# Optimization experiments

Measured on AMD Instinct MI355X. Metric: run time of the kernel, lower is better.

Reference implementation:

```python
import jax, jax.numpy as jnp
import numpy as np

T = 2048
HID = 2048
H = 16
NOPE = 128
ROPE = 64
QKD = NOPE + ROPE  # 192
VD = 128
QLR = 1536
KVLR = 512
IDX_H = 32
IDX_D = 128
TOPK = 512
EPS = 1e-6
SCALING = QKD ** -0.5


def rms_norm(x, w):
    return x * jax.lax.rsqrt(jnp.mean(x * x, axis=-1, keepdims=True) + EPS) * w


def layer_norm(x, g, b):
    mu = jnp.mean(x, axis=-1, keepdims=True)
    var = jnp.mean((x - mu) ** 2, axis=-1, keepdims=True)
    return (x - mu) * jax.lax.rsqrt(var + EPS) * g + b


def apply_rope(x, positions, base=10000.0):
    # non-neox (interleaved) rotary; x: [..., d] with leading token axis
    d = x.shape[-1]
    inv = 1.0 / (base ** (jnp.arange(0, d, 2, dtype=jnp.float32) / d))
    f = positions.astype(jnp.float32)[:, None] * inv  # [T, d/2]
    shp = (x.shape[0],) + (1,) * (x.ndim - 2) + (d // 2,)
    cos, sin = jnp.cos(f).reshape(shp), jnp.sin(f).reshape(shp)
    x1, x2 = x[..., ::2], x[..., 1::2]
    return jnp.stack([x1 * cos - x2 * sin, x1 * sin + x2 * cos], axis=-1).reshape(x.shape)


def setup_inputs() -> dict:
    key = jax.random.key(0)
    ks = jax.random.split(key, 10)
    s = 0.02
    return {
        "positions": jnp.arange(T, dtype=jnp.int64) if jax.config.jax_enable_x64 else jnp.arange(T, dtype=jnp.int32),
        "hidden_states": jax.random.normal(ks[0], (T, HID), jnp.float32),
        "w_qkv_a": jax.random.normal(ks[1], (HID, QLR + KVLR + ROPE), jnp.float32) * s,
        "q_a_ln_w": jnp.ones((QLR,), jnp.float32),
        "w_qb": jax.random.normal(ks[2], (QLR, H * QKD), jnp.float32) * s,
        "kv_a_ln_w": jnp.ones((KVLR,), jnp.float32),
        "w_kvb": jax.random.normal(ks[3], (KVLR, H * (NOPE + VD)), jnp.float32) * s,
        "w_o": jax.random.normal(ks[4], (H * VD, HID), jnp.float32) * s,
        "w_idx_qb": jax.random.normal(ks[5], (QLR, IDX_H * IDX_D), jnp.float32) * s,
        "w_idx_k": jax.random.normal(ks[6], (HID, IDX_D), jnp.float32) * s,
        "idx_k_gamma": jnp.ones((IDX_D,), jnp.float32),
        "idx_k_beta": jnp.zeros((IDX_D,), jnp.float32),
        "w_wproj": jax.random.normal(ks[7], (HID, IDX_H), jnp.float32) * s,
        "b_wproj": jnp.zeros((IDX_H,), jnp.float32),
    }


def _forward(positions, hidden_states, w_qkv_a, q_a_ln_w, w_qb, kv_a_ln_w, w_kvb,
             w_o, w_idx_qb, w_idx_k, idx_k_gamma, idx_k_beta, w_wproj, b_wproj):
    t = hidden_states.shape[0]
    # fused low-rank projections
    qkv = hidden_states @ w_qkv_a
    q_c, kv_c, k_pe = jnp.split(qkv, [QLR, QLR + KVLR], axis=-1)
    q_c = rms_norm(q_c, q_a_ln_w)           # hidden_states_or_q_c
    kv_cn = rms_norm(kv_c, kv_a_ln_w)

    # ---- Indexer (lightning top-k token selection) ----
    qi = (q_c @ w_idx_qb).reshape(t, IDX_H, IDX_D)
    qi_pe, qi_nope = qi[..., :ROPE], qi[..., ROPE:]
    ki = layer_norm(hidden_states @ w_idx_k, idx_k_gamma, idx_k_beta)  # [T, IDX_D]
    ki_pe, ki_nope = ki[..., :ROPE], ki[..., ROPE:]
    qi = jnp.concatenate([apply_rope(qi_pe, positions), qi_nope], axis=-1)
    ki = jnp.concatenate([apply_rope(ki_pe, positions), ki_nope], axis=-1)
    w = (hidden_states @ w_wproj + b_wproj) * (IDX_D ** -0.5) * (IDX_H ** -0.5)  # [T, IDX_H]
    logits = jax.nn.relu(jnp.einsum('thd,sd->ths', qi, ki))   # [T, IDX_H, T]
    score = jnp.einsum('th,ths->ts', w, logits)               # [T, T]
    causal = jnp.tril(jnp.ones((t, t), bool))
    neg = jnp.finfo(score.dtype).min
    score = jnp.where(causal, score, neg)
    _, topk_idx = jax.lax.top_k(score, TOPK)                  # [T, TOPK]
    sel = jnp.zeros((t, t), bool).at[jnp.arange(t)[:, None], topk_idx].set(True)
    mask = causal & sel

    # ---- MLA attention ----
    q = (q_c @ w_qb).reshape(t, H, QKD)
    q_nope, q_pe = q[..., :NOPE], q[..., NOPE:]
    q_pe = apply_rope(q_pe, positions)
    k_pe_r = apply_rope(k_pe, positions)                      # [T, ROPE], shared across heads
    kv = (kv_cn @ w_kvb).reshape(t, H, NOPE + VD)
    k_nope, v = kv[..., :NOPE], kv[..., NOPE:]
    q_full = jnp.concatenate([q_nope, q_pe], axis=-1)         # [T, H, QKD]
    k_full = jnp.concatenate([k_nope, jnp.broadcast_to(k_pe_r[:, None, :], (t, H, ROPE))], axis=-1)
    attn = jnp.einsum('thd,shd->hts', q_full, k_full) * SCALING
    attn = jnp.where(mask[None], attn, neg)
    p = jax.nn.softmax(attn, axis=-1)
    out = jnp.einsum('hts,shv->thv', p, v).reshape(t, H * VD)
    return out @ w_o


def reference(positions, hidden_states, w_qkv_a, q_a_ln_w, w_qb, kv_a_ln_w, w_kvb,
              w_o, w_idx_qb, w_idx_k, idx_k_gamma, idx_k_beta, w_wproj, b_wproj):
    return _forward(positions, hidden_states, w_qkv_a, q_a_ln_w, w_qb, kv_a_ln_w,
                    w_kvb, w_o, w_idx_qb, w_idx_k, idx_k_gamma, idx_k_beta,
                    w_wproj, b_wproj)
```

## Files before the change

### kernel.cpp

```cpp
#include <hip/hip_runtime.h>
#include <cfloat>
#include <cmath>

#define T_    2048
#define HID_  2048
#define QKVN_ 2112
#define QKVX_ 2272
#define QLR_  1536
#define KVLR_ 512
#define ROPE_ 64
#define NOPE_ 128
#define QKD_  192
#define VD_   128
#define H_    16
#define IDXH_ 32
#define IDXD_ 128
#define TOPK_ 512
#define EPS_  1e-6f
#define SCALING_ 0.07216878364870323f

typedef unsigned int u32;
typedef unsigned short u16;
typedef __bf16 bf16x8 __attribute__((ext_vector_type(8)));
typedef _Float16 f16;
typedef f16 f16x8 __attribute__((ext_vector_type(8)));
typedef float f32x4 __attribute__((ext_vector_type(4)));

__device__ __forceinline__ u16 f2bf(float x) {
  u32 u = __float_as_uint(x);
  u32 r = (u + 0x7fffu + ((u >> 16) & 1u)) >> 16;
  return (u16)r;
}
__device__ __forceinline__ float bf2f(u16 h) { return __uint_as_float(((u32)h) << 16); }
__device__ __forceinline__ u32 pack2(float a, float b) { return (u32)f2bf(a) | ((u32)f2bf(b) << 16); }
__device__ __forceinline__ bf16x8 ld8(const void* p) { return *(const bf16x8*)p; }
__device__ __forceinline__ f32x4 mfma16(bf16x8 a, bf16x8 b, f32x4 c) {
  return __builtin_amdgcn_mfma_f32_16x16x32_bf16(a, b, c, 0, 0, 0);
}
__device__ __forceinline__ u16 hbits(f16 h) { union { f16 h; u16 u; } c; c.h = h; return c.u; }
__device__ __forceinline__ u32 hpack(f16 a, f16 b) { return (u32)hbits(a) | ((u32)hbits(b) << 16); }
__device__ __forceinline__ f16x8 ldh8(const void* p) { return *(const f16x8*)p; }
__device__ __forceinline__ f32x4 mfmah(f16x8 a, f16x8 b, f32x4 c) {
  return __builtin_amdgcn_mfma_f32_16x16x32_f16(a, b, c, 0, 0, 0);
}
__device__ __forceinline__ void gload16(const u16* g, u16* l) {
  __builtin_amdgcn_global_load_lds(
      (__attribute__((address_space(1))) void*)(g),
      (__attribute__((address_space(3))) void*)(l), 16, 0, 0);
}

struct TSJob { const float* src; u16* oh; u16* ol; int K; int N; };
__global__ __launch_bounds__(256) void transpose_split_multi(
    TSJob j0, TSJob j1, TSJob j2, TSJob j3) {
  TSJob jb = (blockIdx.z == 0) ? j0 : (blockIdx.z == 1) ? j1 : (blockIdx.z == 2) ? j2 : j3;
  int k0 = blockIdx.y * 64, n0 = blockIdx.x * 64;
  if (k0 >= jb.K || n0 >= jb.N) return;
  __shared__ float t[64][65];
  for (int j = 0; j < 16; ++j) {
    int u = threadIdx.x + 256 * j; int r = u >> 6, c = u & 63;
    t[r][c] = (k0 + r < jb.K && n0 + c < jb.N) ? jb.src[(size_t)(k0 + r) * jb.N + n0 + c] : 0.f;
  }
  __syncthreads();
  for (int j = 0; j < 16; ++j) {
    int u = threadIdx.x + 256 * j; int r = u >> 6, c = u & 63;
    if (n0 + r < jb.N && k0 + c < jb.K) {
      float v = t[c][r];
      f16 h = (f16)v;
      jb.oh[(size_t)(n0 + r) * jb.K + k0 + c] = hbits(h);
      jb.ol[(size_t)(n0 + r) * jb.K + k0 + c] = hbits((f16)(v - (float)h));
    }
  }
}

struct TBJob { const float* src; u16* out; int K; int N; };
__global__ __launch_bounds__(256) void transpose_bf16_multi(TBJob j0, TBJob j1, TBJob j2) {
  TBJob jb = (blockIdx.z == 0) ? j0 : (blockIdx.z == 1) ? j1 : j2;
  int k0 = blockIdx.y * 64, n0 = blockIdx.x * 64;
  if (k0 >= jb.K || n0 >= jb.N) return;
  __shared__ float t[64][65];
  for (int j = 0; j < 16; ++j) {
    int u = threadIdx.x + 256 * j; int r = u >> 6, c = u & 63;
    t[r][c] = (k0 + r < jb.K && n0 + c < jb.N) ? jb.src[(size_t)(k0 + r) * jb.N + n0 + c] : 0.f;
  }
  __syncthreads();
  for (int j = 0; j < 16; ++j) {
    int u = threadIdx.x + 256 * j; int r = u >> 6, c = u & 63;
    if (n0 + r < jb.N && k0 + c < jb.K) jb.out[(size_t)(n0 + r) * jb.K + k0 + c] = f2bf(t[c][r]);
  }
}

__global__ __launch_bounds__(256) void split_f16_k(
    const float* __restrict__ in, u16* __restrict__ hi, u16* __restrict__ lo, long n) {
  for (long i = ((long)blockIdx.x * 256 + threadIdx.x) * 4; i < n; i += (long)gridDim.x * 1024) {
    float4 v = *(const float4*)(in + i);
    f16 a = (f16)v.x, b = (f16)v.y, c = (f16)v.z, d = (f16)v.w;
    *(u32*)(hi + i) = hpack(a, b);
    *(u32*)(hi + i + 2) = hpack(c, d);
    *(u32*)(lo + i) = hpack((f16)(v.x - (float)a), (f16)(v.y - (float)b));
    *(u32*)(lo + i + 2) = hpack((f16)(v.z - (float)c), (f16)(v.w - (float)d));
  }
}

__global__ __launch_bounds__(256) void conv_bf16_k(
    const float* __restrict__ in, u16* __restrict__ out, long n) {
  for (long i = ((long)blockIdx.x * 256 + threadIdx.x) * 4; i < n; i += (long)gridDim.x * 1024) {
    float4 v = *(const float4*)(in + i);
    *(u32*)(out + i) = pack2(v.x, v.y);
    *(u32*)(out + i + 2) = pack2(v.z, v.w);
  }
}

__global__ __launch_bounds__(256) void gemm_hl(
    const u16* __restrict__ Ah_, const u16* __restrict__ Al_, int lda,
    const u16* __restrict__ Bh_, const u16* __restrict__ Bl_, int ldb,
    float* __restrict__ C, int ldc, const float* __restrict__ bias, int bcol0,
    float bscale, int N, int K) {
  __shared__ u32 Ah[128][16], Al[128][16], Bh[128][16], Bl[128][16];
  const int tid = threadIdx.x;
  const int bm = blockIdx.y * 128, bn = blockIdx.x * 128;
  const int wid = tid >> 6, lane = tid & 63, wr = wid >> 1, wc = wid & 1;
  const int lr = lane & 15, lg = lane >> 4;
  const u16* srcb = (wid == 0) ? Ah_ : (wid == 1) ? Al_ : (wid == 2) ? Bh_ : Bl_;
  const int sld = (wid < 2) ? lda : ldb;
  const int rb = (wid < 2) ? bm : bn;
  u16* dst = (u16*)((wid == 0) ? &Ah[0][0] : (wid == 1) ? &Al[0][0]
                                           : (wid == 2) ? &Bh[0][0] : &Bl[0][0]);
  const int rowl = lane >> 2;
  const int offl = (lane & 3) * 8;
  f32x4 acc[4][4] = {};
  for (int k0 = 0; k0 < K; k0 += 32) {
#pragma unroll
    for (int c = 0; c < 8; ++c) {
      int gr = rb + c * 16 + rowl;
      if (wid >= 2) gr = min(gr, N - 1);
      gload16(srcb + (size_t)gr * sld + k0 + offl, dst + c * 512);
    }
    __syncthreads();
    f16x8 ah[4], al[4], bh[4], bl[4];
#pragma unroll
    for (int i = 0; i < 4; ++i) {
      ah[i] = ldh8(&Ah[wr * 64 + i * 16 + lr][lg * 4]);
      al[i] = ldh8(&Al[wr * 64 + i * 16 + lr][lg * 4]);
      bh[i] = ldh8(&Bh[wc * 64 + i * 16 + lr][lg * 4]);
      bl[i] = ldh8(&Bl[wc * 64 + i * 16 + lr][lg * 4]);
    }
#pragma unroll
    for (int i = 0; i < 4; ++i)
#pragma unroll
      for (int jn = 0; jn < 4; ++jn) {
        acc[i][jn] = mfmah(ah[i], bh[jn], acc[i][jn]);
        acc[i][jn] = mfmah(ah[i], bl[jn], acc[i][jn]);
        acc[i][jn] = mfmah(al[i], bh[jn], acc[i][jn]);
      }
    __syncthreads();
  }
#pragma unroll
  for (int i = 0; i < 4; ++i)
#pragma unroll
    for (int jn = 0; jn < 4; ++jn)
#pragma unroll
      for (int j = 0; j < 4; ++j) {
        int row = bm + wr * 64 + i * 16 + lg * 4 + j;
        int col = bn + wc * 64 + jn * 16 + lr;
        if (col < N) {
          float v = acc[i][jn][j];
          if (col >= bcol0) v = (v + bias[col - bcol0]) * bscale;
          C[(size_t)row * ldc + col] = v;
        }
      }
}

template <int CBF16>
__global__ __launch_bounds__(256) void gemm_t(
    const u16* __restrict__ Ab, int lda, long aoz,
    const u16* __restrict__ Bt, int ldb, long boz,
    void* __restrict__ Cp, int ldc, long coz, int N, int K) {
  __shared__ u32 As[128][16], Bs[128][16];
  const int tid = threadIdx.x;
  const int z = blockIdx.z;
  const int bm = blockIdx.y * 128, bn = blockIdx.x * 128;
  const int wid = tid >> 6, lane = tid & 63, wr = wid >> 1, wc = wid & 1;
  const int lr = lane & 15, lg = lane >> 4;
  const u16* A = Ab + aoz * z;
  const u16* B = Bt + boz * z;
  const u16* srcb = (wid < 2) ? A : B;
  const int sld = (wid < 2) ? lda : ldb;
  const int rb = (wid < 2) ? bm : bn;
  u16* dst = (u16*)((wid < 2) ? &As[0][0] : &Bs[0][0]);
  const int ccb = (wid & 1) * 4;
  const int rowl = lane >> 2;
  const int offl = (lane & 3) * 8;
  f32x4 acc[4][4] = {};
  for (int k0 = 0; k0 < K; k0 += 32) {
#pragma unroll
    for (int c = 0; c < 4; ++c) {
      int cc = ccb + c;
      int gr = rb + cc * 16 + rowl;
      if (wid >= 2) gr = min(gr, N - 1);
      gload16(srcb + (size_t)gr * sld + k0 + offl, dst + cc * 512);
    }
    __syncthreads();
    bf16x8 af[4], bf[4];
#pragma unroll
    for (int i = 0; i < 4; ++i) {
      af[i] = ld8(&As[wr * 64 + i * 16 + lr][lg * 4]);
      bf[i] = ld8(&Bs[wc * 64 + i * 16 + lr][lg * 4]);
    }
#pragma unroll
    for (int i = 0; i < 4; ++i)
#pragma unroll
      for (int jn = 0; jn < 4; ++jn)
        acc[i][jn] = mfma16(af[i], bf[jn], acc[i][jn]);
    __syncthreads();
  }
#pragma unroll
  for (int i = 0; i < 4; ++i)
#pragma unroll
    for (int jn = 0; jn < 4; ++jn)
#pragma unroll
      for (int j = 0; j < 4; ++j) {
        int row = bm + wr * 64 + i * 16 + lg * 4 + j;
        int col = bn + wc * 64 + jn * 16 + lr;
        if (col < N) {
          if (CBF16) ((u16*)Cp)[coz * z + (size_t)row * ldc + col] = f2bf(acc[i][jn][j]);
          else ((float*)Cp)[coz * z + (size_t)row * ldc + col] = acc[i][jn][j];
        }
      }
}

__global__ __launch_bounds__(256) void rmsnorm_kernel(
    const float* __restrict__ qkvx, const float* __restrict__ qw,
    const float* __restrict__ kvw, u16* __restrict__ qcb,
    u16* __restrict__ qch, u16* __restrict__ qcl, u16* __restrict__ kv_cn) {
  const int t = blockIdx.x, tid = threadIdx.x;
  const float* row = qkvx + (size_t)t * QKVX_;
  __shared__ float red[256];
  float ss = 0.f;
  for (int i = tid; i < QLR_; i += 256) { float v = row[i]; ss += v * v; }
  red[tid] = ss; __syncthreads();
  for (int s = 128; s; s >>= 1) { if (tid < s) red[tid] += red[tid + s]; __syncthreads(); }
  float scl = 1.0f / sqrtf(red[0] / (float)QLR_ + EPS_);
  for (int i = tid; i < QLR_; i += 256) {
    float val = row[i] * scl * qw[i];
    qcb[(size_t)t * QLR_ + i] = f2bf(val);
    f16 h = (f16)val;
    qch[(size_t)t * QLR_ + i] = hbits(h);
    qcl[(size_t)t * QLR_ + i] = hbits((f16)(val - (float)h));
  }
  __syncthreads();
  ss = 0.f;
  for (int i = tid; i < KVLR_; i += 256) { float v = row[QLR_ + i]; ss += v * v; }
  red[tid] = ss; __syncthreads();
  for (int s = 128; s; s >>= 1) { if (tid < s) red[tid] += red[tid + s]; __syncthreads(); }
  scl = 1.0f / sqrtf(red[0] / (float)KVLR_ + EPS_);
  for (int i = tid; i < KVLR_; i += 256)
    kv_cn[(size_t)t * KVLR_ + i] = f2bf(row[QLR_ + i] * scl * kvw[i]);
}

__device__ __forceinline__ void rope_pair(float pos, int j, float& x0, float& x1) {
  float inv = powf(10000.f, -(float)j * (1.f / 32.f));
  float f = pos * inv;
  float c = cosf(f), s = sinf(f);
  float a = x0, b = x1;
  x0 = a * c - b * s;
  x1 = a * s + b * c;
}

__global__ __launch_bounds__(256) void rope_qi_split_kernel(
    const float* __restrict__ qi, u16* __restrict__ qih, u16* __restrict__ qil) {
  const int t = blockIdx.x, tid = threadIdx.x;
  float pos = (float)t;
  const float* src = qi + (size_t)t * (IDXH_ * IDXD_);
  u16* dh = qih + (size_t)t * (IDXH_ * IDXD_);
  u16* dl = qil + (size_t)t * (IDXH_ * IDXD_);
  for (int p = tid; p < IDXH_ * IDXD_ / 2; p += 256) {
    int d = p & 63;
    float x0 = src[2 * p], x1 = src[2 * p + 1];
    if (d < 32) rope_pair(pos, d, x0, x1);
    f16 h0 = (f16)x0, h1 = (f16)x1;
    *(u32*)(dh + 2 * p) = hpack(h0, h1);
    *(u32*)(dl + 2 * p) = hpack((f16)(x0 - (float)h0), (f16)(x1 - (float)h1));
  }
}

__global__ __launch_bounds__(256) void rope_q_bf_kernel(u16* __restrict__ qfb) {
  const int t = blockIdx.x, tid = threadIdx.x;
  float pos = (float)t;
  for (int idx = tid; idx < H_ * 32; idx += 256) {
    int hh = idx / 32, j = idx % 32;
    u16* p = qfb + (size_t)t * (H_ * QKD_) + hh * QKD_ + NOPE_ + 2 * j;
    float x0 = bf2f(p[0]), x1 = bf2f(p[1]);
    rope_pair(pos, j, x0, x1);
    p[0] = f2bf(x0); p[1] = f2bf(x1);
  }
}

__global__ __launch_bounds__(64) void rope_kpe_kernel(
    const float* __restrict__ qkvx, u16* __restrict__ kper) {
  const int t = blockIdx.x, tid = threadIdx.x;
  if (tid >= 32) return;
  float pos = (float)t;
  const float* p = qkvx + (size_t)t * QKVX_ + (QLR_ + KVLR_);
  float x0 = p[2 * tid], x1 = p[2 * tid + 1];
  rope_pair(pos, tid, x0, x1);
  kper[(size_t)t * ROPE_ + 2 * tid] = f2bf(x0);
  kper[(size_t)t * ROPE_ + 2 * tid + 1] = f2bf(x1);
}

__global__ __launch_bounds__(128) void ki_ln_rope_kernel(
    const float* __restrict__ qkvx, const float* __restrict__ gamma,
    const float* __restrict__ beta, u16* __restrict__ kih, u16* __restrict__ kil) {
  const int t = blockIdx.x, tid = threadIdx.x;
  __shared__ float x[128];
  __shared__ float red[128];
  float v = qkvx[(size_t)t * QKVX_ + QKVN_ + tid];
  red[tid] = v; __syncthreads();
  for (int s = 64; s; s >>= 1) { if (tid < s) red[tid] += red[tid + s]; __syncthreads(); }
  float mu = red[0] / 128.f;
  __syncthreads();
  float d = v - mu;
  red[tid] = d * d; __syncthreads();
  for (int s = 64; s; s >>= 1) { if (tid < s) red[tid] += red[tid + s]; __syncthreads(); }
  float var = red[0] / 128.f;
  float y = d * (1.0f / sqrtf(var + EPS_)) * gamma[tid] + beta[tid];
  x[tid] = y; __syncthreads();
  float pos = (float)t;
  if (tid < 32) {
    float x0 = x[2 * tid], x1 = x[2 * tid + 1];
    rope_pair(pos, tid, x0, x1);
    x[2 * tid] = x0; x[2 * tid + 1] = x1;
  }
  __syncthreads();
  float fv = x[tid];
  f16 h = (f16)fv;
  kih[(size_t)t * IDXD_ + tid] = hbits(h);
  kil[(size_t)t * IDXD_ + tid] = hbits((f16)(fv - (float)h));
}

__global__ __launch_bounds__(256) void score_mfma(
    const u16* __restrict__ qih, const u16* __restrict__ qil,
    const u16* __restrict__ kih, const u16* __restrict__ kil,
    const float* __restrict__ wgt, int ldw, float* __restrict__ score) {
  const int s0 = blockIdx.x * 64, t0 = blockIdx.y * 64;
  if (s0 > t0 + 63) return;
  __shared__ u32 Kh[64][68], Kl[64][68], Qh[64][68], Ql[64][68];
  __shared__ float wts[64][33];
  const int tid = threadIdx.x;
  const int wid = tid >> 6, lane = tid & 63, wr = wid >> 1, wc = wid & 1;
  const int lr = lane & 15, lg = lane >> 4;
#pragma unroll
  for (int j = 0; j < 4; ++j) {
    int u = tid + 256 * j; int row = u >> 4, p = u & 15;
    *(uint4*)&Kh[row][p * 4] = *(const uint4*)(kih + (size_t)(s0 + row) * IDXD_ + p * 8);
    *(uint4*)&Kl[row][p * 4] = *(const uint4*)(kil + (size_t)(s0 + row) * IDXD_ + p * 8);
  }
#pragma unroll
  for (int j = 0; j < 8; ++j) {
    int u = tid + 256 * j; int r = u >> 5, c = u & 31;
    wts[r][c] = wgt[(size_t)(t0 + r) * ldw + c];
  }
  __syncthreads();
  f16x8 bh[2][4], bl[2][4];
#pragma unroll
  for (int ni = 0; ni < 2; ++ni)
#pragma unroll
    for (int kb = 0; kb < 4; ++kb) {
      bh[ni][kb] = ldh8(&Kh[wc * 32 + ni * 16 + lr][kb * 16 + lg * 4]);
      bl[ni][kb] = ldh8(&Kl[wc * 32 + ni * 16 + lr][kb * 16 + lg * 4]);
    }
  f32x4 fin[2][2] = {};
  for (int h = 0; h < IDXH_; ++h) {
#pragma unroll
    for (int j = 0; j < 4; ++j) {
      int u = tid + 256 * j; int row = u >> 4, p = u & 15;
      size_t g = (size_t)(t0 + row) * (IDXH_ * IDXD_) + h * IDXD_ + p * 8;
      *(uint4*)&Qh[row][p * 4] = *(const uint4*)(qih + g);
      *(uint4*)&Ql[row][p * 4] = *(const uint4*)(qil + g);
    }
    __syncthreads();
    f32x4 acch[2][2] = {};
#pragma unroll
    for (int kb = 0; kb < 4; ++kb) {
      f16x8 ah0 = ldh8(&Qh[wr * 32 + lr][kb * 16 + lg * 4]);
      f16x8 ah1 = ldh8(&Qh[wr * 32 + 16 + lr][kb * 16 + lg * 4]);
      f16x8 al0 = ldh8(&Ql[wr * 32 + lr][kb * 16 + lg * 4]);
      f16x8 al1 = ldh8(&Ql[wr * 32 + 16 + lr][kb * 16 + lg * 4]);
#pragma unroll
      for (int ni = 0; ni < 2; ++ni) {
        acch[0][ni] = mfmah(ah0, bh[ni][kb], acch[0][ni]);
        acch[0][ni] = mfmah(ah0, bl[ni][kb], acch[0][ni]);
        acch[0][ni] = mfmah(al0, bh[ni][kb], acch[0][ni]);
        acch[1][ni] = mfmah(ah1, bh[ni][kb], acch[1][ni]);
        acch[1][ni] = mfmah(ah1, bl[ni][kb], acch[1][ni]);
        acch[1][ni] = mfmah(al1, bh[ni][kb], acch[1][ni]);
      }
    }
#pragma unroll
    for (int mi = 0; mi < 2; ++mi)
#pragma unroll
      for (int j = 0; j < 4; ++j) {
        float w = wts[wr * 32 + mi * 16 + lg * 4 + j][h];
        fin[mi][0][j] += w * fmaxf(acch[mi][0][j], 0.f);
        fin[mi][1][j] += w * fmaxf(acch[mi][1][j], 0.f);
      }
    __syncthreads();
  }
#pragma unroll
  for (int mi = 0; mi < 2; ++mi)
#pragma unroll
    for (int ni = 0; ni < 2; ++ni)
#pragma unroll
      for (int j = 0; j < 4; ++j) {
        int row = t0 + wr * 32 + mi * 16 + lg * 4 + j;
        int col = s0 + wc * 32 + ni * 16 + lr;
        score[(size_t)row * T_ + col] = fin[mi][ni][j];
      }
}

__global__ __launch_bounds__(256) void topk_kernel(
    const float* __restrict__ score, int* __restrict__ selidx,
    int* __restrict__ selcnt) {
  const int t = blockIdx.x;
  const int L = t + 1;
  const int tid = threadIdx.x;
  if (L <= TOPK_) {
    for (int j = tid; j < TOPK_; j += 256)
      selidx[(size_t)t * TOPK_ + j] = (j < L) ? j : 0;
    if (tid == 0) selcnt[t] = L;
    return;
  }
  __shared__ unsigned u[T_];
  __shared__ unsigned hist[16];
  __shared__ unsigned sprefix;
  __shared__ int sk;
  __shared__ int part[256];
  for (int i = tid; i < T_; i += 256) {
    float v = (i < L) ? score[(size_t)t * T_ + i] : -FLT_MAX;
    unsigned b = __float_as_uint(v);
    u[i] = (b & 0x80000000u) ? ~b : (b | 0x80000000u);
  }
  if (tid == 0) { sprefix = 0u; sk = TOPK_; }
  __syncthreads();
  for (int pass = 0; pass < 8; ++pass) {
    const int shift = 28 - 4 * pass;
    if (tid < 16) hist[tid] = 0u;
    __syncthreads();
    unsigned pfx = sprefix;
    for (int i = tid; i < L; i += 256) {
      unsigned val = u[i];
      bool match = (pass == 0) || ((val >> (shift + 4)) == pfx);
      if (match) atomicAdd(&hist[(val >> shift) & 15u], 1u);
    }
    __syncthreads();
    if (tid == 0) {
      int k = sk; unsigned cum = 0u; int bsel = 0;
      for (int bb = 15; bb >= 0; --bb) {
        if (cum + hist[bb] >= (unsigned)k) { bsel = bb; sk = k - (int)cum; break; }
        cum += hist[bb];
      }
      sprefix = (sprefix << 4) | (unsigned)bsel;
    }
    __syncthreads();
  }
  const unsigned thr = sprefix;
  const int kEq = sk;
  const int base = tid * 8;
  int eqloc[8]; int esum = 0;
  for (int r = 0; r < 8; ++r) {
    int i = base + r;
    int f = (i < L && u[i] == thr) ? 1 : 0;
    eqloc[r] = esum; esum += f;
  }
  part[tid] = esum; __syncthreads();
  for (int off = 1; off < 256; off <<= 1) {
    int v = (tid >= off) ? part[tid - off] : 0;
    __syncthreads();
    part[tid] += v;
    __syncthreads();
  }
  const int ebase = (tid > 0) ? part[tid - 1] : 0;
  __syncthreads();
  int sloc[8], selflag[8]; int ssum = 0;
  for (int r = 0; r < 8; ++r) {
    int i = base + r;
    int f = 0;
    if (i < L) {
      unsigned ui = u[i];
      if (ui > thr) f = 1;
      else if (ui == thr && (ebase + eqloc[r]) < kEq) f = 1;
    }
    selflag[r] = f; sloc[r] = ssum; ssum += f;
  }
  part[tid] = ssum; __syncthreads();
  for (int off = 1; off < 256; off <<= 1) {
    int v = (tid >= off) ? part[tid - off] : 0;
    __syncthreads();
    part[tid] += v;
    __syncthreads();
  }
  const int sbase = (tid > 0) ? part[tid - 1] : 0;
  for (int r = 0; r < 8; ++r)
    if (selflag[r]) selidx[(size_t)t * TOPK_ + sbase + sloc[r]] = base + r;
  if (tid == 0) selcnt[t] = TOPK_;
}

__global__ __launch_bounds__(256, 3) void attn_mla_kernel(
    const u16* __restrict__ qeff, const u16* __restrict__ qfb,
    const u16* __restrict__ kvcn, const u16* __restrict__ kper,
    const int* __restrict__ selidx, const int* __restrict__ selcnt,
    u16* __restrict__ Olat) {
  const int t = blockIdx.x;
  const int tid = threadIdx.x;
  const int wid = tid >> 6, lane = tid & 63;
  const int lr = lane & 15, lg = lane >> 4;
  __shared__ int sidxs[512];
  __shared__ u16 Pb[16][520];
  __shared__ u32 Vp[4][16][128];
  __shared__ float redm[4][16];
  __shared__ float reds[4][16];
  const int cnt = selcnt[t];
  for (int j = tid; j < 512; j += 256) sidxs[j] = selidx[(size_t)t * TOPK_ + j];
  __syncthreads();

  int srow[8];
  const u16* kb8[8];
  const u16* kp8[8];
#pragma unroll
  for (int m = 0; m < 8; ++m) {
    srow[m] = sidxs[wid * 128 + m * 16 + lr];
    kb8[m] = kvcn + (size_t)srow[m] * 512 + lg * 8;
    kp8[m] = kper + (size_t)srow[m] * 64 + lg * 8;
  }
  const u16* qe = qeff + (size_t)t * (H_ * 512) + lr * 512 + lg * 8;
  const u16* qp = qfb + (size_t)t * (H_ * QKD_) + lr * QKD_ + NOPE_ + lg * 8;
  f32x4 lgv[8] = {};
  bf16x8 kc[8];
#pragma unroll
  for (int m = 0; m < 8; ++m) kc[m] = ld8(kb8[m]);
#pragma unroll
  for (int kb = 0; kb < 16; ++kb) {
    bf16x8 qfk = ld8(qe + kb * 32);
    bf16x8 kn[8];
#pragma unroll
    for (int m = 0; m < 8; ++m)
      kn[m] = (kb < 15) ? ld8(kb8[m] + (kb + 1) * 32) : ld8(kp8[m]);
#pragma unroll
    for (int m = 0; m < 8; ++m) lgv[m] = mfma16(kc[m], qfk, lgv[m]);
#pragma unroll
    for (int m = 0; m < 8; ++m) kc[m] = kn[m];
  }
  {
    bf16x8 qfk = ld8(qp);
    bf16x8 kn[8];
#pragma unroll
    for (int m = 0; m < 8; ++m) kn[m] = ld8(kp8[m] + 32);
#pragma unroll
    for (int m = 0; m < 8; ++m) lgv[m] = mfma16(kc[m], qfk, lgv[m]);
#pragma unroll
    for (int m = 0; m < 8; ++m) kc[m] = kn[m];
  }
  {
    bf16x8 qfk = ld8(qp + 32);
#pragma unroll
    for (int m = 0; m < 8; ++m) lgv[m] = mfma16(kc[m], qfk, lgv[m]);
  }

  float mx = -FLT_MAX;
#pragma unroll
  for (int m = 0; m < 8; ++m)
#pragma unroll
    for (int j = 0; j < 4; ++j) {
      int slot = wid * 128 + m * 16 + lg * 4 + j;
      float v = (slot < cnt) ? lgv[m][j] * SCALING_ : -FLT_MAX;
      lgv[m][j] = v;
      mx = fmaxf(mx, v);
    }
  mx = fmaxf(mx, __shfl_xor(mx, 16));
  mx = fmaxf(mx, __shfl_xor(mx, 32));
  if (lane < 16) redm[wid][lane] = mx;
  __syncthreads();
  float hm = fmaxf(fmaxf(redm[0][lr], redm[1][lr]), fmaxf(redm[2][lr], redm[3][lr]));
  float sm = 0.f;
#pragma unroll
  for (int m = 0; m < 8; ++m)
#pragma unroll
    for (int j = 0; j < 4; ++j) {
      int slot = wid * 128 + m * 16 + lg * 4 + j;
      float e = (slot < cnt) ? expf(lgv[m][j] - hm) : 0.f;
      lgv[m][j] = e; sm += e;
    }
  sm += __shfl_xor(sm, 16);
  sm += __shfl_xor(sm, 32);
  if (lane < 16) reds[wid][lane] = sm;
  __syncthreads();
  float inv = 1.f / (reds[0][lr] + reds[1][lr] + reds[2][lr] + reds[3][lr]);
#pragma unroll
  for (int m = 0; m < 8; ++m) {
    int sl = wid * 128 + m * 16 + lg * 4;
    *(u32*)&Pb[lr][sl] = pack2(lgv[m][0] * inv, lgv[m][1] * inv);
    *(u32*)&Pb[lr][sl + 2] = pack2(lgv[m][2] * inv, lgv[m][3] * inv);
  }
  __syncthreads();

  const int pl = lane >> 4;
  const int gq = lane & 15;
  const u16* vsrc = kvcn + wid * 128 + gq * 8;
  f32x4 oacc[8] = {};
  uint4 ra[4], rb[4];
#pragma unroll
  for (int s = 0; s < 4; ++s) {
    int p = s * 4 + pl;
    ra[s] = *(const uint4*)(vsrc + (size_t)sidxs[2 * p] * 512);
    rb[s] = *(const uint4*)(vsrc + (size_t)sidxs[2 * p + 1] * 512);
  }
  for (int c = 0; c < 16; ++c) {
#pragma unroll
    for (int s = 0; s < 4; ++s) {
      int p = s * 4 + pl;
      int col = (gq * 8) ^ ((s & 3) << 3);
      const u16* A = (const u16*)&ra[s];
      const u16* B = (const u16*)&rb[s];
      u32 w[8];
#pragma unroll
      for (int j = 0; j < 8; ++j) w[j] = (u32)A[j] | ((u32)B[j] << 16);
      *(uint4*)&Vp[wid][p][col] = make_uint4(w[0], w[1], w[2], w[3]);
      *(uint4*)&Vp[wid][p][col + 4] = make_uint4(w[4], w[5], w[6], w[7]);
    }
    if (c < 15) {
#pragma unroll
      for (int s = 0; s < 4; ++s) {
        int p = s * 4 + pl;
        ra[s] = *(const uint4*)(vsrc + (size_t)sidxs[(c + 1) * 32 + 2 * p] * 512);
        rb[s] = *(const uint4*)(vsrc + (size_t)sidxs[(c + 1) * 32 + 2 * p + 1] * 512);
      }
    }
    bf16x8 pa = ld8(&Pb[lr][c * 32 + lg * 8]);
    union BB { u32 u[4]; bf16x8 v; };
    BB bb[8];
#pragma unroll
    for (int C = 0; C < 8; ++C) {
      int col = (C * 16 + lr) ^ (lg << 3);
#pragma unroll
      for (int e = 0; e < 4; ++e)
        bb[C].u[e] = Vp[wid][lg * 4 + e][col];
    }
    __builtin_amdgcn_s_setprio(1);
#pragma unroll
    for (int C = 0; C < 8; ++C) oacc[C] = mfma16(pa, bb[C].v, oacc[C]);
    __builtin_amdgcn_s_setprio(0);
  }
#pragma unroll
  for (int C = 0; C < 8; ++C)
#pragma unroll
    for (int j = 0; j < 4; ++j) {
      int h = lg * 4 + j;
      Olat[(size_t)t * (H_ * 512) + h * 512 + wid * 128 + C * 16 + lr] = f2bf(oacc[C][j]);
    }
}

extern "C" void kernel_launch(void* const* d_in, const int* in_sizes, int n_in,
                              void* d_out, int out_size, void* d_ws, size_t ws_size,
                              hipStream_t stream) {
  const float* hidden    = (const float*)d_in[1];
  const float* w_qkv_a   = (const float*)d_in[2];
  const float* q_a_ln_w  = (const float*)d_in[3];
  const float* w_qb      = (const float*)d_in[4];
  const float* kv_a_ln_w = (const float*)d_in[5];
  const float* w_kvb     = (const float*)d_in[6];
  const float* w_o       = (const float*)d_in[7];
  const float* w_idx_qb  = (const float*)d_in[8];
  const float* w_idx_k   = (const float*)d_in[9];
  const float* idx_g     = (const float*)d_in[10];
  const float* idx_b     = (const float*)d_in[11];
  const float* w_wproj   = (const float*)d_in[12];
  const float* b_wproj   = (const float*)d_in[13];

  char* W = (char*)d_ws;
  size_t o = 0;
  auto alloc = [&](size_t bytes) { void* p = W + o; o += (bytes + 255) & ~(size_t)255; return p; };
  u16* qcb     = (u16*)alloc((size_t)T_ * QLR_ * 2);
  u16* kv_cn   = (u16*)alloc((size_t)T_ * KVLR_ * 2);
  u16* kper    = (u16*)alloc((size_t)T_ * ROPE_ * 2);
  int* selidx  = (int*)alloc((size_t)T_ * TOPK_ * 4);
  int* selcnt  = (int*)alloc((size_t)T_ * 4);
  u16* kih     = (u16*)alloc((size_t)T_ * IDXD_ * 2);
  u16* kil     = (u16*)alloc((size_t)T_ * IDXD_ * 2);
  u16* hidh    = (u16*)alloc((size_t)T_ * HID_ * 2);
  u16* hidl    = (u16*)alloc((size_t)T_ * HID_ * 2);
  u16* qch     = (u16*)alloc((size_t)T_ * QLR_ * 2);
  u16* qcl     = (u16*)alloc((size_t)T_ * QLR_ * 2);
  u16* wiqh    = (u16*)alloc((size_t)(IDXH_ * IDXD_) * QLR_ * 2);
  u16* wiql    = (u16*)alloc((size_t)(IDXH_ * IDXD_) * QLR_ * 2);
  u16* qih     = qch;
  u16* qil     = qch + (size_t)T_ * IDXH_ * IDXD_;
  float* qi    = (float*)alloc((size_t)T_ * IDXH_ * IDXD_ * 4);
  u16* qeff    = (u16*)qi;
  float* score = (float*)alloc((size_t)T_ * T_ * 4);
  u16* qfb     = (u16*)score;
  u16* attno   = (u16*)score;
  u16* wcath   = (u16*)alloc((size_t)QKVX_ * HID_ * 2);
  u16* wcatl   = (u16*)alloc((size_t)QKVX_ * HID_ * 2);
  float* qkvx  = (float*)alloc((size_t)T_ * QKVX_ * 4);
  u16* Olat    = wcath;
  u16* wqbt    = (u16*)alloc((size_t)(H_ * QKD_) * QLR_ * 2);
  u16* wkvb    = (u16*)alloc((size_t)KVLR_ * (H_ * 256) * 2);
  u16* wkvbt   = (u16*)alloc((size_t)(H_ * 256) * KVLR_ * 2);
  u16* wot     = (u16*)alloc((size_t)(H_ * VD_) * HID_ * 2);

  dim3 blk(256);
  auto g2 = [](int M, int N, int Z) { return dim3((N + 127) / 128, M / 128, Z); };

  {
    TSJob j0{w_qkv_a, wcath, wcatl, HID_, QKVN_};
    TSJob j1{w_idx_qb, wiqh, wiql, QLR_, IDXH_ * IDXD_};
    TSJob j2{w_idx_k, wcath + (size_t)QKVN_ * HID_, wcatl + (size_t)QKVN_ * HID_, HID_, IDXD_};
    TSJob j3{w_wproj, wcath + (size_t)(QKVN_ + IDXD_) * HID_, wcatl + (size_t)(QKVN_ + IDXD_) * HID_, HID_, IDXH_};
    transpose_split_multi<<<dim3(64, 32, 4), blk, 0, stream>>>(j0, j1, j2, j3);
  }
  {
    TBJob j0{w_qb, wqbt, QLR_, H_ * QKD_};
    TBJob j1{w_kvb, wkvbt, KVLR_, H_ * 256};
    TBJob j2{w_o, wot, H_ * VD_, HID_};
    transpose_bf16_multi<<<dim3(64, 32, 3), blk, 0, stream>>>(j0, j1, j2);
  }
  split_f16_k<<<2048, blk, 0, stream>>>(hidden, hidh, hidl, (long)T_ * HID_);
  conv_bf16_k<<<2048, blk, 0, stream>>>(w_kvb, wkvb, (long)KVLR_ * H_ * 256);

  gemm_hl<<<g2(T_, QKVX_, 1), blk, 0, stream>>>(
      hidh, hidl, HID_, wcath, wcatl, HID_, qkvx, QKVX_,
      b_wproj, QKVN_ + IDXD_, 0.015625f, QKVX_, HID_);
  rmsnorm_kernel<<<T_, blk, 0, stream>>>(qkvx, q_a_ln_w, kv_a_ln_w, qcb, qch, qcl, kv_cn);
  rope_kpe_kernel<<<T_, 64, 0, stream>>>(qkvx, kper);
  ki_ln_rope_kernel<<<T_, 128, 0, stream>>>(qkvx, idx_g, idx_b, kih, kil);

  gemm_hl<<<g2(T_, IDXH_ * IDXD_, 1), blk, 0, stream>>>(
      qch, qcl, QLR_, wiqh, wiql, QLR_, qi, IDXH_ * IDXD_,
      nullptr, 1 << 30, 1.f, IDXH_ * IDXD_, QLR_);
  rope_qi_split_kernel<<<T_, blk, 0, stream>>>(qi, qih, qil);

  score_mfma<<<dim3(32, 32), blk, 0, stream>>>(qih, qil, kih, kil,
                                               qkvx + QKVN_ + IDXD_, QKVX_, score);
  topk_kernel<<<T_, blk, 0, stream>>>(score, selidx, selcnt);

  gemm_t<1><<<g2(T_, H_ * QKD_, 1), blk, 0, stream>>>(qcb, QLR_, 0, wqbt, QLR_, 0, qfb, H_ * QKD_, 0, H_ * QKD_, QLR_);
  rope_q_bf_kernel<<<T_, blk, 0, stream>>>(qfb);
  gemm_t<1><<<g2(T_, 512, H_), blk, 0, stream>>>(qfb, H_ * QKD_, QKD_, wkvb, H_ * 256, 256, qeff, H_ * 512, 512, 512, NOPE_);
  attn_mla_kernel<<<T_, blk, 0, stream>>>(qeff, qfb, kv_cn, kper, selidx, selcnt, Olat);
  gemm_t<1><<<g2(T_, VD_, H_), blk, 0, stream>>>(Olat, H_ * 512, 512, wkvbt + 128 * 512, KVLR_, 256 * 512, attno, H_ * VD_, VD_, VD_, 512);
  gemm_t<0><<<g2(T_, HID_, 1), blk, 0, stream>>>(attno, H_ * VD_, 0, wot, H_ * VD_, 0, d_out, HID_, 0, HID_, H_ * VD_);
}
```

Measured before the change: 712.5 us.

## Precompute RoPE cos/sin table and stage attention keys through LDS

Adds a kernel that precomputes a per-position cos/sin table once, and the four RoPE kernels now read from it instead of calling powf/sinf/cosf per element. Separately, the MLA attention score loop now gathers each selected key row into shared memory with global_load_lds, waits on it, then reads MFMA operands from LDS, and preloads all query fragments into registers. The shared buffer is reused for the V staging. The key gather was previously register-pipelined, while the new version waits on vmcnt(0) every k-block, which serialises load and compute and uses more registers for the query fragments.

```diff
diff --git a/kernel.cpp b/kernel.cpp
--- a/kernel.cpp
+++ b/kernel.cpp
@@ -47,6 +47,20 @@
   __builtin_amdgcn_global_load_lds(
       (__attribute__((address_space(1))) void*)(g),
       (__attribute__((address_space(3))) void*)(l), 16, 0, 0);
+}
+
+__global__ __launch_bounds__(256) void rope_tab_kernel(float2* __restrict__ tab) {
+  int i = blockIdx.x * 256 + threadIdx.x;
+  if (i >= T_ * 32) return;
+  int t = i >> 5, j = i & 31;
+  float inv = powf(10000.f, -(float)j * (1.f / 32.f));
+  float f = (float)t * inv;
+  tab[i] = make_float2(cosf(f), sinf(f));
+}
+__device__ __forceinline__ void rope_apply(float2 cs, float& x0, float& x1) {
+  float a = x0, b = x1;
+  x0 = a * cs.x - b * cs.y;
+  x1 = a * cs.y + b * cs.x;
 }
 
 struct TSJob { const float* src; u16* oh; u16* ol; int K; int N; };
@@ -257,59 +271,51 @@
     kv_cn[(size_t)t * KVLR_ + i] = f2bf(row[QLR_ + i] * scl * kvw[i]);
 }
 
-__device__ __forceinline__ void rope_pair(float pos, int j, float& x0, float& x1) {
-  float inv = powf(10000.f, -(float)j * (1.f / 32.f));
-  float f = pos * inv;
-  float c = cosf(f), s = sinf(f);
-  float a = x0, b = x1;
-  x0 = a * c - b * s;
-  x1 = a * s + b * c;
-}
-
 __global__ __launch_bounds__(256) void rope_qi_split_kernel(
-    const float* __restrict__ qi, u16* __restrict__ qih, u16* __restrict__ qil) {
+    const float* __restrict__ qi, const float2* __restrict__ tab,
+    u16* __restrict__ qih, u16* __restrict__ qil) {
   const int t = blockIdx.x, tid = threadIdx.x;
-  float pos = (float)t;
   const float* src = qi + (size_t)t * (IDXH_ * IDXD_);
   u16* dh = qih + (size_t)t * (IDXH_ * IDXD_);
   u16* dl = qil + (size_t)t * (IDXH_ * IDXD_);
   for (int p = tid; p < IDXH_ * IDXD_ / 2; p += 256) {
     int d = p & 63;
     float x0 = src[2 * p], x1 = src[2 * p + 1];
-    if (d < 32) rope_pair(pos, d, x0, x1);
+    if (d < 32) rope_apply(tab[t * 32 + d], x0, x1);
     f16 h0 = (f16)x0, h1 = (f16)x1;
     *(u32*)(dh + 2 * p) = hpack(h0, h1);
     *(u32*)(dl + 2 * p) = hpack((f16)(x0 - (float)h0), (f16)(x1 - (float)h1));
   }
 }
 
-__global__ __launch_bounds__(256) void rope_q_bf_kernel(u16* __restrict__ qfb) {
+__global__ __launch_bounds__(256) void rope_q_bf_kernel(
+    u16* __restrict__ qfb, const float2* __restrict__ tab) {
   const int t = blockIdx.x, tid = threadIdx.x;
-  float pos = (float)t;
   for (int idx = tid; idx < H_ * 32; idx += 256) {
     int hh = idx / 32, j = idx % 32;
     u16* p = qfb + (size_t)t * (H_ * QKD_) + hh * QKD_ + NOPE_ + 2 * j;
     float x0 = bf2f(p[0]), x1 = bf2f(p[1]);
-    rope_pair(pos, j, x0, x1);
+    rope_apply(tab[t * 32 + j], x0, x1);
     p[0] = f2bf(x0); p[1] = f2bf(x1);
   }
 }
 
 __global__ __launch_bounds__(64) void rope_kpe_kernel(
-    const float* __restrict__ qkvx, u16* __restrict__ kper) {
+    const float* __restrict__ qkvx, const float2* __restrict__ tab,
+    u16* __restrict__ kper) {
   const int t = blockIdx.x, tid = threadIdx.x;
   if (tid >= 32) return;
-  float pos = (float)t;
   const float* p = qkvx + (size_t)t * QKVX_ + (QLR_ + KVLR_);
   float x0 = p[2 * tid], x1 = p[2 * tid + 1];
-  rope_pair(pos, tid, x0, x1);
+  rope_apply(tab[t * 32 + tid], x0, x1);
   kper[(size_t)t * ROPE_ + 2 * tid] = f2bf(x0);
   kper[(size_t)t * ROPE_ + 2 * tid + 1] = f2bf(x1);
 }
 
 __global__ __launch_bounds__(128) void ki_ln_rope_kernel(
     const float* __restrict__ qkvx, const float* __restrict__ gamma,
-    const float* __restrict__ beta, u16* __restrict__ kih, u16* __restrict__ kil) {
+    const float* __restrict__ beta, const float2* __restrict__ tab,
+    u16* __restrict__ kih, u16* __restrict__ kil) {
   const int t = blockIdx.x, tid = threadIdx.x;
   __shared__ float x[128];
   __shared__ float red[128];
@@ -324,10 +330,9 @@
   float var = red[0] / 128.f;
   float y = d * (1.0f / sqrtf(var + EPS_)) * gamma[tid] + beta[tid];
   x[tid] = y; __syncthreads();
-  float pos = (float)t;
   if (tid < 32) {
     float x0 = x[2 * tid], x1 = x[2 * tid + 1];
-    rope_pair(pos, tid, x0, x1);
+    rope_apply(tab[t * 32 + tid], x0, x1);
     x[2 * tid] = x0; x[2 * tid + 1] = x1;
   }
   __syncthreads();
@@ -515,54 +520,49 @@
   const int lr = lane & 15, lg = lane >> 4;
   __shared__ int sidxs[512];
   __shared__ u16 Pb[16][520];
-  __shared__ u32 Vp[4][16][128];
+  __shared__ u16 SB[4][4096];
   __shared__ float redm[4][16];
   __shared__ float reds[4][16];
   const int cnt = selcnt[t];
   for (int j = tid; j < 512; j += 256) sidxs[j] = selidx[(size_t)t * TOPK_ + j];
   __syncthreads();
 
-  int srow[8];
-  const u16* kb8[8];
-  const u16* kp8[8];
-#pragma unroll
-  for (int m = 0; m < 8; ++m) {
-    srow[m] = sidxs[wid * 128 + m * 16 + lr];
-    kb8[m] = kvcn + (size_t)srow[m] * 512 + lg * 8;
-    kp8[m] = kper + (size_t)srow[m] * 64 + lg * 8;
-  }
+  const int kl = lane >> 2;
+  const int pc = (lane & 3) * 8;
+  int skey[8];
+#pragma unroll
+  for (int j = 0; j < 8; ++j) skey[j] = sidxs[wid * 128 + j * 16 + kl];
+  u16* ksw = &SB[wid][0];
+
   const u16* qe = qeff + (size_t)t * (H_ * 512) + lr * 512 + lg * 8;
   const u16* qp = qfb + (size_t)t * (H_ * QKD_) + lr * QKD_ + NOPE_ + lg * 8;
+  bf16x8 qf[18];
+#pragma unroll
+  for (int kb = 0; kb < 16; ++kb) qf[kb] = ld8(qe + kb * 32);
+  qf[16] = ld8(qp);
+  qf[17] = ld8(qp + 32);
+
   f32x4 lgv[8] = {};
-  bf16x8 kc[8];
-#pragma unroll
-  for (int m = 0; m < 8; ++m) kc[m] = ld8(kb8[m]);
-#pragma unroll
-  for (int kb = 0; kb < 16; ++kb) {
-    bf16x8 qfk = ld8(qe + kb * 32);
-    bf16x8 kn[8];
-#pragma unroll
-    for (int m = 0; m < 8; ++m)
-      kn[m] = (kb < 15) ? ld8(kb8[m] + (kb + 1) * 32) : ld8(kp8[m]);
-#pragma unroll
-    for (int m = 0; m < 8; ++m) lgv[m] = mfma16(kc[m], qfk, lgv[m]);
-#pragma unroll
-    for (int m = 0; m < 8; ++m) kc[m] = kn[m];
-  }
-  {
-    bf16x8 qfk = ld8(qp);
-    bf16x8 kn[8];
-#pragma unroll
-    for (int m = 0; m < 8; ++m) kn[m] = ld8(kp8[m] + 32);
-#pragma unroll
-    for (int m = 0; m < 8; ++m) lgv[m] = mfma16(kc[m], qfk, lgv[m]);
-#pragma unroll
-    for (int m = 0; m < 8; ++m) kc[m] = kn[m];
-  }
-  {
-    bf16x8 qfk = ld8(qp + 32);
-#pragma unroll
-    for (int m = 0; m < 8; ++m) lgv[m] = mfma16(kc[m], qfk, lgv[m]);
+#pragma unroll
+  for (int kb = 0; kb < 18; ++kb) {
+    if (kb < 16) {
+#pragma unroll
+      for (int j = 0; j < 8; ++j)
+        gload16(kvcn + (size_t)skey[j] * 512 + kb * 32 + pc, ksw + j * 512);
+    } else {
+#pragma unroll
+      for (int j = 0; j < 8; ++j)
+        gload16(kper + (size_t)skey[j] * 64 + (kb - 16) * 32 + pc, ksw + j * 512);
+    }
+    asm volatile("s_waitcnt vmcnt(0)" ::: "memory");
+    __builtin_amdgcn_sched_barrier(0);
+#pragma unroll
+    for (int m = 0; m < 8; ++m) {
+      bf16x8 kf = ld8(ksw + (m * 16 + lr) * 32 + lg * 8);
+      lgv[m] = mfma16(kf, qf[kb], lgv[m]);
+    }
+    asm volatile("s_waitcnt lgkmcnt(0)" ::: "memory");
+    __builtin_amdgcn_sched_barrier(0);
   }
 
   float mx = -FLT_MAX;
@@ -602,6 +602,7 @@
   }
   __syncthreads();
 
+  u32* vpw = (u32*)&SB[wid][0];
   const int pl = lane >> 4;
   const int gq = lane & 15;
   const u16* vsrc = kvcn + wid * 128 + gq * 8;
@@ -623,8 +624,8 @@
       u32 w[8];
 #pragma unroll
       for (int j = 0; j < 8; ++j) w[j] = (u32)A[j] | ((u32)B[j] << 16);
-      *(uint4*)&Vp[wid][p][col] = make_uint4(w[0], w[1], w[2], w[3]);
-      *(uint4*)&Vp[wid][p][col + 4] = make_uint4(w[4], w[5], w[6], w[7]);
+      *(uint4*)&vpw[p * 128 + col] = make_uint4(w[0], w[1], w[2], w[3]);
+      *(uint4*)&vpw[p * 128 + col + 4] = make_uint4(w[4], w[5], w[6], w[7]);
     }
     if (c < 15) {
 #pragma unroll
@@ -642,7 +643,7 @@
       int col = (C * 16 + lr) ^ (lg << 3);
 #pragma unroll
       for (int e = 0; e < 4; ++e)
-        bb[C].u[e] = Vp[wid][lg * 4 + e][col];
+        bb[C].u[e] = vpw[(lg * 4 + e) * 128 + col];
     }
     __builtin_amdgcn_s_setprio(1);
 #pragma unroll
@@ -687,6 +688,7 @@
   u16* kil     = (u16*)alloc((size_t)T_ * IDXD_ * 2);
   u16* hidh    = (u16*)alloc((size_t)T_ * HID_ * 2);
   u16* hidl    = (u16*)alloc((size_t)T_ * HID_ * 2);
+  float2* rtab = (float2*)alloc((size_t)T_ * 32 * 8);
   u16* qch     = (u16*)alloc((size_t)T_ * QLR_ * 2);
   u16* qcl     = (u16*)alloc((size_t)T_ * QLR_ * 2);
   u16* wiqh    = (u16*)alloc((size_t)(IDXH_ * IDXD_) * QLR_ * 2);
@@ -710,6 +712,7 @@
   dim3 blk(256);
   auto g2 = [](int M, int N, int Z) { return dim3((N + 127) / 128, M / 128, Z); };
 
+  rope_tab_kernel<<<(T_ * 32 + 255) / 256, blk, 0, stream>>>(rtab);
   {
     TSJob j0{w_qkv_a, wcath, wcatl, HID_, QKVN_};
     TSJob j1{w_idx_qb, wiqh, wiql, QLR_, IDXH_ * IDXD_};
@@ -730,20 +733,20 @@
       hidh, hidl, HID_, wcath, wcatl, HID_, qkvx, QKVX_,
       b_wproj, QKVN_ + IDXD_, 0.015625f, QKVX_, HID_);
   rmsnorm_kernel<<<T_, blk, 0, stream>>>(qkvx, q_a_ln_w, kv_a_ln_w, qcb, qch, qcl, kv_cn);
-  rope_kpe_kernel<<<T_, 64, 0, stream>>>(qkvx, kper);
-  ki_ln_rope_kernel<<<T_, 128, 0, stream>>>(qkvx, idx_g, idx_b, kih, kil);
+  rope_kpe_kernel<<<T_, 64, 0, stream>>>(qkvx, rtab, kper);
+  ki_ln_rope_kernel<<<T_, 128, 0, stream>>>(qkvx, idx_g, idx_b, rtab, kih, kil);
 
   gemm_hl<<<g2(T_, IDXH_ * IDXD_, 1), blk, 0, stream>>>(
       qch, qcl, QLR_, wiqh, wiql, QLR_, qi, IDXH_ * IDXD_,
       nullptr, 1 << 30, 1.f, IDXH_ * IDXD_, QLR_);
-  rope_qi_split_kernel<<<T_, blk, 0, stream>>>(qi, qih, qil);
+  rope_qi_split_kernel<<<T_, blk, 0, stream>>>(qi, rtab, qih, qil);
 
   score_mfma<<<dim3(32, 32), blk, 0, stream>>>(qih, qil, kih, kil,
                                                qkvx + QKVN_ + IDXD_, QKVX_, score);
   topk_kernel<<<T_, blk, 0, stream>>>(score, selidx, selcnt);
 
   gemm_t<1><<<g2(T_, H_ * QKD_, 1), blk, 0, stream>>>(qcb, QLR_, 0, wqbt, QLR_, 0, qfb, H_ * QKD_, 0, H_ * QKD_, QLR_);
-  rope_q_bf_kernel<<<T_, blk, 0, stream>>>(qfb);
+  rope_q_bf_kernel<<<T_, blk, 0, stream>>>(qfb, rtab);
   gemm_t<1><<<g2(T_, 512, H_), blk, 0, stream>>>(qfb, H_ * QKD_, QKD_, wkvb, H_ * 256, 256, qeff, H_ * 512, 512, 512, NOPE_);
   attn_mla_kernel<<<T_, blk, 0, stream>>>(qeff, qfb, kv_cn, kper, selidx, selcnt, Olat);
   gemm_t<1><<<g2(T_, VD_, H_), blk, 0, stream>>>(Olat, H_ * 512, 512, wkvbt + 128 * 512, KVLR_, 256 * 512, attno, H_ * VD_, VD_, VD_, 512);
```

After: 666.5 us. 1.07x faster.
